# Kernel optimization log

Hardware: AMD Instinct MI355X
Metric: run time of the kernel (lower is better)

Reference implementation:

```python
import jax, jax.numpy as jnp
import numpy as np

N_NODES = 50000   # number of graph nodes
N_EDGES = 800000  # avg degree 16
D = 128           # in_dim == all hdims -> residual active every layer
L = 3             # len(cfg['hdims'])


def setup_inputs() -> dict:
    key = jax.random.key(0)
    ks = jax.random.split(key, 8)
    scale = 1.0 / np.sqrt(D)
    x = jax.random.normal(ks[0], (N_NODES, D), dtype=jnp.float32)
    edge_index = jax.random.randint(ks[1], (2, N_EDGES), 0, N_NODES, dtype=jnp.int32)
    in_fc_w = jax.random.normal(ks[2], (D, D), dtype=jnp.float32) * scale
    in_fc_b = jnp.zeros((D,), dtype=jnp.float32)
    # GraphConv per layer: lin_rel (with bias) applied to aggregated neighbors,
    # lin_root (no bias) applied to self features. All layers are DxD -> stack.
    w_rel = jax.random.normal(ks[3], (L, D, D), dtype=jnp.float32) * scale
    b_rel = jnp.zeros((L, D), dtype=jnp.float32)
    w_root = jax.random.normal(ks[4], (L, D, D), dtype=jnp.float32) * scale
    return {"x": x, "edge_index": edge_index, "in_fc_w": in_fc_w,
            "in_fc_b": in_fc_b, "w_rel": w_rel, "b_rel": b_rel, "w_root": w_root}


def reference(x, edge_index, in_fc_w, in_fc_b, w_rel, b_rel, w_root):
    src, dst = edge_index[0], edge_index[1]
    h = x @ in_fc_w + in_fc_b                     # in_fc
    for l in range(L):                            # fixed small layer count
        # GraphConv, aggr='add': gather source feats, scatter-add to targets
        agg = jax.ops.segment_sum(h[src], dst, num_segments=N_NODES)  # [N, D]
        out = agg @ w_rel[l] + b_rel[l] + h @ w_root[l]
        out = jax.nn.relu(out)
        h = out + h                               # residual (dims match)
    return h
```

## Files before the change

### kernel.cpp

```cpp
#include <hip/hip_runtime.h>
#include <hip/hip_bf16.h>


constexpr int D = 128;
constexpr int NB_SHIFT = 7;
constexpr int BCAP = 2560;
constexpr int STRIDE = 3456;
constexpr int CHUNK = 2048;
constexpr int NRANGE = 16;

typedef __attribute__((ext_vector_type(8))) short bf16x8;
typedef __attribute__((ext_vector_type(4))) float f32x4;
typedef __attribute__((ext_vector_type(4))) unsigned int u32x4;

__device__ inline unsigned short f2bf(float f) {
    unsigned int u = __builtin_bit_cast(unsigned int, f);
    u += 0x7FFFu + ((u >> 16) & 1u);
    return (unsigned short)(u >> 16);
}
__device__ inline float bf2f(unsigned short v) {
    return __builtin_bit_cast(float, (unsigned int)v << 16);
}
__device__ inline float bf2f_lo(unsigned int v) {
    return __builtin_bit_cast(float, v << 16);
}
__device__ inline float bf2f_hi(unsigned int v) {
    return __builtin_bit_cast(float, v & 0xFFFF0000u);
}

__global__ __launch_bounds__(256) void prep(
    const float* __restrict__ x, const float* __restrict__ fc_w,
    const float* __restrict__ w_rel, const float* __restrict__ w_root,
    unsigned short* __restrict__ xb, unsigned short* __restrict__ Wp,
    int* __restrict__ cursor, unsigned short* __restrict__ hb0,
    unsigned short* __restrict__ hb1, int n4, int NB, int N)
{
    int blk = blockIdx.x;
    const int nconv = (n4 + 255) / 256;
    if (blk < nconv) {
        int i = blk * 256 + threadIdx.x;
        if (i < n4) {
            float4 v = ((const float4*)x)[i];
            ushort4 o;
            o.x = f2bf(v.x); o.y = f2bf(v.y); o.z = f2bf(v.z); o.w = f2bf(v.w);
            ((ushort4*)xb)[i] = o;
        }
        return;
    }
    blk -= nconv;
    if (blk < 56) {
        int idx = blk * 256 + threadIdx.x;
        int mat  = idx >> 11;
        int rem  = idx & 2047;
        int tn   = rem >> 8;
        int ks   = (rem >> 6) & 3;
        int lane = rem & 63;
        const float* w = (mat == 0) ? fc_w
                       : (mat <= 3) ? w_rel  + (size_t)(mat - 1) * D * D
                                    : w_root + (size_t)(mat - 4) * D * D;
        unsigned short* wp = Wp + (size_t)mat * D * D + (size_t)rem * 8;
        int kbase = ks * 32 + (lane >> 4) * 8;
        int col   = tn * 16 + (lane & 15);
        #pragma unroll
        for (int j = 0; j < 8; ++j)
            wp[j] = f2bf(w[(size_t)(kbase + j) * D + col]);
        return;
    }
    blk -= 56;
    const int ncb = (NB + 255) / 256;
    if (blk < ncb) {
        int i = blk * 256 + threadIdx.x;
        if (i < NB) cursor[i] = 0;
        return;
    }
    if (threadIdx.x < 64)
        ((unsigned int*)(hb0 + (size_t)N * D))[threadIdx.x] = 0u;
    else if (threadIdx.x < 128)
        ((unsigned int*)(hb1 + (size_t)N * D))[threadIdx.x - 64] = 0u;
}

__global__ __launch_bounds__(256) void gemm_mfma(
    const unsigned short* __restrict__ A1, const unsigned short* __restrict__ W1p,
    const float* __restrict__ bias, unsigned short* __restrict__ hb_out, int N)
{
    const int tid  = threadIdx.x;
    const int wave = tid >> 6;
    const int lane = tid & 63;
    const int row0 = blockIdx.x * 64 + wave * 16;
    const int mrow = lane & 15;
    const int kgrp = lane >> 4;

    f32x4 acc[8];
    #pragma unroll
    for (int t = 0; t < 8; ++t) acc[t] = (f32x4){0.f, 0.f, 0.f, 0.f};

    int arow = row0 + mrow; if (arow >= N) arow = N - 1;
    const size_t abase = (size_t)arow * D + kgrp * 8;

    #pragma unroll
    for (int ks = 0; ks < 4; ++ks) {
        bf16x8 a1 = *(const bf16x8*)(A1 + abase + ks * 32);
        #pragma unroll
        for (int tn = 0; tn < 8; ++tn) {
            bf16x8 b = *(const bf16x8*)(W1p + ((size_t)((tn * 4 + ks) * 64 + lane) * 8));
            acc[tn] = __builtin_amdgcn_mfma_f32_16x16x32_bf16(a1, b, acc[tn], 0, 0, 0);
        }
    }

    const int r0 = row0 + kgrp * 4;
    #pragma unroll
    for (int tn = 0; tn < 8; ++tn) {
        const int col = tn * 16 + mrow;
        const float bv = bias[col];
        #pragma unroll
        for (int reg = 0; reg < 4; ++reg) {
            int r = r0 + reg;
            if (r < N) hb_out[(size_t)r * D + col] = f2bf(acc[tn][reg] + bv);
        }
    }
}

__global__ __launch_bounds__(256) void layer_fused(
    const unsigned short* __restrict__ hb_in, const int* __restrict__ eb,
    const unsigned int* __restrict__ sorted_off,
    const unsigned short* __restrict__ Wrel, const unsigned short* __restrict__ Wroot,
    const float* __restrict__ bias,
    unsigned short* hb_out, float* out_f32, int N)
{
    __shared__ unsigned short aggt[16][136];

    const int tid   = threadIdx.x;
    const int wave  = tid >> 6;
    const int lane  = tid & 63;
    const int node0 = blockIdx.x * 16;

    {
        const int g = lane >> 4;
        const int c = lane & 15;
        const int n = node0 + wave * 4 + g;

        float acc[8];
        #pragma unroll
        for (int q = 0; q < 8; ++q) acc[q] = 0.f;

        if (n < N) {
            const int2 be = ((const int2*)eb)[n];
            int j = be.x;
            const int e = be.y;
            const unsigned int c16 = (unsigned int)c * 16u;
            const char* hb = (const char*)hb_in;
            if (j < e) {
                u32x4 iA = *(const u32x4*)(sorted_off + j);
                u32x4 iB = *(const u32x4*)(sorted_off + j + 4);
                for (;;) {
                    u32x4 v0 = *(const u32x4*)(hb + (iA[0] + c16));
                    u32x4 v1 = *(const u32x4*)(hb + (iA[1] + c16));
                    u32x4 v2 = *(const u32x4*)(hb + (iA[2] + c16));
                    u32x4 v3 = *(const u32x4*)(hb + (iA[3] + c16));
                    u32x4 v4 = *(const u32x4*)(hb + (iB[0] + c16));
                    u32x4 v5 = *(const u32x4*)(hb + (iB[1] + c16));
                    u32x4 v6 = *(const u32x4*)(hb + (iB[2] + c16));
                    u32x4 v7 = *(const u32x4*)(hb + (iB[3] + c16));
                    const bool more = (j + 8 < e);
                    u32x4 nA, nB;
                    if (more) {
                        nA = *(const u32x4*)(sorted_off + j + 8);
                        nB = *(const u32x4*)(sorted_off + j + 12);
                    }
                    #pragma unroll
                    for (int q = 0; q < 4; ++q) {
                        acc[2 * q]     += ((bf2f_lo(v0[q]) + bf2f_lo(v1[q])) + (bf2f_lo(v2[q]) + bf2f_lo(v3[q])))
                                        + ((bf2f_lo(v4[q]) + bf2f_lo(v5[q])) + (bf2f_lo(v6[q]) + bf2f_lo(v7[q])));
                        acc[2 * q + 1] += ((bf2f_hi(v0[q]) + bf2f_hi(v1[q])) + (bf2f_hi(v2[q]) + bf2f_hi(v3[q])))
                                        + ((bf2f_hi(v4[q]) + bf2f_hi(v5[q])) + (bf2f_hi(v6[q]) + bf2f_hi(v7[q])));
                    }
                    if (!more) break;
                    iA = nA; iB = nB; j += 8;
                }
            }
        }
        u32x4 o;
        #pragma unroll
        for (int q = 0; q < 4; ++q)
            o[q] = (unsigned int)f2bf(acc[2 * q]) |
                   ((unsigned int)f2bf(acc[2 * q + 1]) << 16);
        *(u32x4*)&aggt[wave * 4 + g][c * 8] = o;
    }
    __syncthreads();

    const int mrow = lane & 15;
    const int kgrp = lane >> 4;

    f32x4 acc2[2];
    acc2[0] = (f32x4){0.f, 0.f, 0.f, 0.f};
    acc2[1] = (f32x4){0.f, 0.f, 0.f, 0.f};

    int arow = node0 + mrow; if (arow >= N) arow = N - 1;
    const size_t abase = (size_t)arow * D + kgrp * 8;

    #pragma unroll
    for (int ks = 0; ks < 4; ++ks) {
        bf16x8 a1 = *(const bf16x8*)&aggt[mrow][ks * 32 + kgrp * 8];
        bf16x8 a2 = *(const bf16x8*)(hb_in + abase + ks * 32);
        #pragma unroll
        for (int t = 0; t < 2; ++t) {
            const int tn = wave * 2 + t;
            bf16x8 b1 = *(const bf16x8*)(Wrel  + ((size_t)((tn * 4 + ks) * 64 + lane) * 8));
            acc2[t] = __builtin_amdgcn_mfma_f32_16x16x32_bf16(a1, b1, acc2[t], 0, 0, 0);
            bf16x8 b2 = *(const bf16x8*)(Wroot + ((size_t)((tn * 4 + ks) * 64 + lane) * 8));
            acc2[t] = __builtin_amdgcn_mfma_f32_16x16x32_bf16(a2, b2, acc2[t], 0, 0, 0);
        }
    }

    const int r0 = node0 + kgrp * 4;
    #pragma unroll
    for (int t = 0; t < 2; ++t) {
        const int tn  = wave * 2 + t;
        const int col = tn * 16 + mrow;
        const float bv = bias[col];
        #pragma unroll
        for (int reg = 0; reg < 4; ++reg) {
            int r = r0 + reg;
            if (r < N) {
                float z = fmaxf(acc2[t][reg] + bv, 0.f);
                float o = z + bf2f(hb_in[(size_t)r * D + col]);
                if (out_f32 != nullptr) out_f32[(size_t)r * D + col] = o;
                else                    hb_out[(size_t)r * D + col] = f2bf(o);
            }
        }
    }
}

__global__ __launch_bounds__(256) void bucket_scatter(
    const int* __restrict__ src, const int* __restrict__ dst,
    unsigned int* __restrict__ entries, int* __restrict__ cursor, int E, int NB)
{
    __shared__ unsigned int   stage[CHUNK];
    __shared__ unsigned short bslot[CHUNK];
    __shared__ int lhist[512];
    __shared__ int lscan[512];
    __shared__ int lgbase[512];
    __shared__ int lcur[512];
    __shared__ int sh[256];

    const int base  = blockIdx.x * CHUNK;
    const int count = min(CHUNK, E - base);
    const int tid   = threadIdx.x;

    for (int i = tid; i < 512; i += 256) { lhist[i] = 0; lcur[i] = 0; }
    __syncthreads();

    for (int i = tid; i < count; i += 256)
        atomicAdd(&lhist[dst[base + i] >> NB_SHIFT], 1);
    __syncthreads();

    int v2 = lhist[2 * tid] + lhist[2 * tid + 1];
    sh[tid] = v2;
    __syncthreads();
    #pragma unroll
    for (int off = 1; off < 256; off <<= 1) {
        int t = (tid >= off) ? sh[tid - off] : 0;
        __syncthreads();
        sh[tid] += t;
        __syncthreads();
    }
    int excl2 = sh[tid] - v2;
    lscan[2 * tid]     = excl2;
    lscan[2 * tid + 1] = excl2 + lhist[2 * tid];
    __syncthreads();

    for (int t = tid; t < 512; t += 256) {
        int c = (t < NB) ? lhist[t] : 0;
        lgbase[t] = (c > 0) ? atomicAdd(&cursor[t], c) : 0;
    }
    __syncthreads();

    for (int i = tid; i < count; i += 256) {
        int d = dst[base + i];
        int s = src[base + i];
        int b = d >> NB_SHIFT;
        int p = atomicAdd(&lcur[b], 1);
        int slot = lscan[b] + p;
        stage[slot] = ((unsigned int)(d & ((1 << NB_SHIFT) - 1)) << 16) | (unsigned int)s;
        bslot[slot] = (unsigned short)b;
    }
    __syncthreads();

    for (int i = tid; i < count; i += 256) {
        int b   = bslot[i];
        int off = i - lscan[b] + lgbase[b];
        if (off < BCAP) entries[(size_t)b * BCAP + off] = stage[i];
    }
}

__global__ __launch_bounds__(256) void bucket_sort(
    const unsigned int* __restrict__ entries, const int* __restrict__ cursor,
    unsigned int* __restrict__ sorted_off, int* __restrict__ eb,
    int N, int NB, float inv_range, unsigned int zero_off)
{
    const int b   = blockIdx.x;
    const int tid = threadIdx.x;

    __shared__ int nhist[128 * NRANGE];
    __shared__ int nscan[128 * NRANGE];
    __shared__ int ncur[128 * NRANGE];
    __shared__ int nbase[129];
    __shared__ int sh[256];
    __shared__ unsigned int svals[STRIDE];

    const int cnt = min(cursor[b], BCAP);

    for (int i = tid; i < 128 * NRANGE; i += 256) { nhist[i] = 0; ncur[i] = 0; }
    __syncthreads();

    const unsigned int* ebase = entries + (size_t)b * BCAP;
    for (int i = tid; i < cnt; i += 256) {
        unsigned int e = ebase[i];
        int s = (int)(e & 0xFFFFu);
        int r = (int)((float)s * inv_range); if (r > NRANGE - 1) r = NRANGE - 1;
        atomicAdd(&nhist[(int)((e >> 16) << 4) | r], 1);
    }
    __syncthreads();

    int c4 = 0, pc = 0;
    if (tid < 128) {
        int s = 0;
        #pragma unroll
        for (int q = 0; q < NRANGE; ++q) s += nhist[NRANGE * tid + q];
        c4 = s;
        pc = (c4 + 7) & ~7;
    }
    sh[tid] = (tid < 128) ? pc : 0;
    __syncthreads();
    #pragma unroll
    for (int off = 1; off < 128; off <<= 1) {
        int t = (tid >= off && tid < 128) ? sh[tid - off] : 0;
        __syncthreads();
        if (tid < 128) sh[tid] += t;
        __syncthreads();
    }
    if (tid < 128) nbase[tid] = sh[tid] - pc;
    if (tid == 127) nbase[128] = sh[127];
    __syncthreads();
    const int padded_total = nbase[128];

    if (tid < 128) {
        int base = nbase[tid];
        int run = base;
        #pragma unroll
        for (int q = 0; q < NRANGE; ++q) {
            nscan[NRANGE * tid + q] = run;
            run += nhist[NRANGE * tid + q];
        }
        int nn = (b << NB_SHIFT) + tid;
        if (nn < N) {
            eb[2 * nn]     = b * STRIDE + base;
            eb[2 * nn + 1] = b * STRIDE + base + pc;
        }
    }
    for (int i = tid; i < padded_total; i += 256) svals[i] = zero_off;
    __syncthreads();

    for (int i = tid; i < cnt; i += 256) {
        unsigned int e = ebase[i];
        int s = (int)(e & 0xFFFFu);
        int r = (int)((float)s * inv_range); if (r > NRANGE - 1) r = NRANGE - 1;
        int key = (int)((e >> 16) << 4) | r;
        int p = atomicAdd(&ncur[key], 1);
        svals[nscan[key] + p] = ((unsigned int)s) << 8;
    }
    __syncthreads();

    unsigned int* obase = sorted_off + (size_t)b * STRIDE;
    for (int i = tid; i < padded_total; i += 256) obase[i] = svals[i];
}

extern "C" void kernel_launch(void* const* d_in, const int* in_sizes, int n_in,
                              void* d_out, int out_size, void* d_ws, size_t ws_size,
                              hipStream_t stream)
{
    const float* x      = (const float*)d_in[0];
    const int*   ei     = (const int*)  d_in[1];
    const float* fc_w   = (const float*)d_in[2];
    const float* fc_b   = (const float*)d_in[3];
    const float* w_rel  = (const float*)d_in[4];
    const float* b_rel  = (const float*)d_in[5];
    const float* w_root = (const float*)d_in[6];
    float* out = (float*)d_out;

    const int N = in_sizes[0] / D;
    const int E = in_sizes[1] / 2;
    const int* src = ei;
    const int* dst = ei + E;
    const int NB = (N + (1 << NB_SHIFT) - 1) >> NB_SHIFT;

    char* p = (char*)d_ws;
    unsigned short* hb0 = (unsigned short*)p;  p += (size_t)(N + 1) * D * sizeof(unsigned short);
    unsigned short* hb1 = (unsigned short*)p;  p += (size_t)(N + 1) * D * sizeof(unsigned short);
    unsigned short* Wp  = (unsigned short*)p;  p += (size_t)7 * D * D * sizeof(unsigned short);
    unsigned int* sorted_off = (unsigned int*)p;  p += (size_t)NB * STRIDE * sizeof(unsigned int);
    int* eb     = (int*)p;                     p += (size_t)2 * N * sizeof(int);
    int* cursor = (int*)p;                     p += (size_t)NB * sizeof(int);
    unsigned int* entries = (unsigned int*)d_out;

    unsigned short* Wp_in   = Wp;
    unsigned short* Wp_rel  = Wp + (size_t)1 * D * D;
    unsigned short* Wp_root = Wp + (size_t)4 * D * D;
    unsigned short* xb = hb1;

    const int n4 = N * D / 4;
    const int gemm_blocks  = (N + 63) / 64;
    const int layer_blocks = (N + 15) / 16;
    const int prep_blocks  = (n4 + 255) / 256 + 56 + (NB + 255) / 256 + 1;

    prep<<<prep_blocks, 256, 0, stream>>>(x, fc_w, w_rel, w_root, xb, Wp, cursor,
                                          hb0, hb1, n4, NB, N);

    bucket_scatter<<<(E + CHUNK - 1) / CHUNK, 256, 0, stream>>>(
        src, dst, entries, cursor, E, NB);
    bucket_sort<<<NB, 256, 0, stream>>>(
        entries, cursor, sorted_off, eb, N, NB, (float)NRANGE / (float)N,
        ((unsigned int)N) << 8);

    gemm_mfma<<<gemm_blocks, 256, 0, stream>>>(xb, Wp_in, fc_b, hb0, N);

    unsigned short* hin  = hb0;
    unsigned short* hout = hb1;
    for (int l = 0; l < 3; ++l) {
        layer_fused<<<layer_blocks, 256, 0, stream>>>(
            hin, eb, sorted_off,
            Wp_rel + (size_t)l * D * D, Wp_root + (size_t)l * D * D,
            b_rel + (size_t)l * D,
            (l == 2) ? nullptr : hout,
            (l == 2) ? out : nullptr, N);
        unsigned short* t = hin; hin = hout; hout = t;
    }
}
```

Baseline: 238.3 us.

## Fuse input GEMM with edge bucket scatter and convert x to bf16 in-kernel

Removes the separate fp32-to-bf16 conversion pass over x from the prep kernel; the input GEMM now loads fp32 x directly and converts in registers. The GEMM is merged into the bucket_scatter launch as extra blocks, so the independent edge-bucketing and input projection run concurrently in one launch. This drops a full write and reread of the bf16 copy of x and one kernel launch. The merged kernel carries the scatter's shared-memory footprint in every block, which may lower occupancy for the GEMM blocks.

```diff
diff --git a/kernel.cpp b/kernel.cpp
--- a/kernel.cpp
+++ b/kernel.cpp
@@ -29,25 +29,12 @@
 }
 
 __global__ __launch_bounds__(256) void prep(
-    const float* __restrict__ x, const float* __restrict__ fc_w,
-    const float* __restrict__ w_rel, const float* __restrict__ w_root,
-    unsigned short* __restrict__ xb, unsigned short* __restrict__ Wp,
+    const float* __restrict__ fc_w, const float* __restrict__ w_rel,
+    const float* __restrict__ w_root, unsigned short* __restrict__ Wp,
     int* __restrict__ cursor, unsigned short* __restrict__ hb0,
-    unsigned short* __restrict__ hb1, int n4, int NB, int N)
+    unsigned short* __restrict__ hb1, int NB, int N)
 {
     int blk = blockIdx.x;
-    const int nconv = (n4 + 255) / 256;
-    if (blk < nconv) {
-        int i = blk * 256 + threadIdx.x;
-        if (i < n4) {
-            float4 v = ((const float4*)x)[i];
-            ushort4 o;
-            o.x = f2bf(v.x); o.y = f2bf(v.y); o.z = f2bf(v.z); o.w = f2bf(v.w);
-            ((ushort4*)xb)[i] = o;
-        }
-        return;
-    }
-    blk -= nconv;
     if (blk < 56) {
         int idx = blk * 256 + threadIdx.x;
         int mat  = idx >> 11;
@@ -79,14 +66,77 @@
         ((unsigned int*)(hb1 + (size_t)N * D))[threadIdx.x - 64] = 0u;
 }
 
-__global__ __launch_bounds__(256) void gemm_mfma(
-    const unsigned short* __restrict__ A1, const unsigned short* __restrict__ W1p,
+__global__ __launch_bounds__(256) void scatter_gemm(
+    const int* __restrict__ src, const int* __restrict__ dst,
+    unsigned int* __restrict__ entries, int* __restrict__ cursor, int E, int NB, int NS,
+    const float* __restrict__ x, const unsigned short* __restrict__ W1p,
     const float* __restrict__ bias, unsigned short* __restrict__ hb_out, int N)
 {
-    const int tid  = threadIdx.x;
+    const int tid = threadIdx.x;
+
+    if (blockIdx.x < (unsigned)NS) {
+        __shared__ unsigned int   stage[CHUNK];
+        __shared__ unsigned short bslot[CHUNK];
+        __shared__ int lhist[512];
+        __shared__ int lscan[512];
+        __shared__ int lgbase[512];
+        __shared__ int lcur[512];
+        __shared__ int sh[256];
+
+        const int base  = blockIdx.x * CHUNK;
+        const int count = min(CHUNK, E - base);
+
+        for (int i = tid; i < 512; i += 256) { lhist[i] = 0; lcur[i] = 0; }
+        __syncthreads();
+
+        for (int i = tid; i < count; i += 256)
+            atomicAdd(&lhist[dst[base + i] >> NB_SHIFT], 1);
+        __syncthreads();
+
+        int v2 = lhist[2 * tid] + lhist[2 * tid + 1];
+        sh[tid] = v2;
+        __syncthreads();
+        #pragma unroll
+        for (int off = 1; off < 256; off <<= 1) {
+            int t = (tid >= off) ? sh[tid - off] : 0;
+            __syncthreads();
+            sh[tid] += t;
+            __syncthreads();
+        }
+        int excl2 = sh[tid] - v2;
+        lscan[2 * tid]     = excl2;
+        lscan[2 * tid + 1] = excl2 + lhist[2 * tid];
+        __syncthreads();
+
+        for (int t = tid; t < 512; t += 256) {
+            int c = (t < NB) ? lhist[t] : 0;
+            lgbase[t] = (c > 0) ? atomicAdd(&cursor[t], c) : 0;
+        }
+        __syncthreads();
+
+        for (int i = tid; i < count; i += 256) {
+            int d = dst[base + i];
+            int s = src[base + i];
+            int b = d >> NB_SHIFT;
+            int p = atomicAdd(&lcur[b], 1);
+            int slot = lscan[b] + p;
+            stage[slot] = ((unsigned int)(d & ((1 << NB_SHIFT) - 1)) << 16) | (unsigned int)s;
+            bslot[slot] = (unsigned short)b;
+        }
+        __syncthreads();
+
+        for (int i = tid; i < count; i += 256) {
+            int b   = bslot[i];
+            int off = i - lscan[b] + lgbase[b];
+            if (off < BCAP) entries[(size_t)b * BCAP + off] = stage[i];
+        }
+        return;
+    }
+
+    const int blk  = blockIdx.x - NS;
     const int wave = tid >> 6;
     const int lane = tid & 63;
-    const int row0 = blockIdx.x * 64 + wave * 16;
+    const int row0 = blk * 64 + wave * 16;
     const int mrow = lane & 15;
     const int kgrp = lane >> 4;
 
@@ -95,11 +145,17 @@
     for (int t = 0; t < 8; ++t) acc[t] = (f32x4){0.f, 0.f, 0.f, 0.f};
 
     int arow = row0 + mrow; if (arow >= N) arow = N - 1;
-    const size_t abase = (size_t)arow * D + kgrp * 8;
+    const float* xr = x + (size_t)arow * D + kgrp * 8;
 
     #pragma unroll
     for (int ks = 0; ks < 4; ++ks) {
-        bf16x8 a1 = *(const bf16x8*)(A1 + abase + ks * 32);
+        float4 f0 = *(const float4*)(xr + ks * 32);
+        float4 f1 = *(const float4*)(xr + ks * 32 + 4);
+        bf16x8 a1;
+        a1[0] = (short)f2bf(f0.x); a1[1] = (short)f2bf(f0.y);
+        a1[2] = (short)f2bf(f0.z); a1[3] = (short)f2bf(f0.w);
+        a1[4] = (short)f2bf(f1.x); a1[5] = (short)f2bf(f1.y);
+        a1[6] = (short)f2bf(f1.z); a1[7] = (short)f2bf(f1.w);
         #pragma unroll
         for (int tn = 0; tn < 8; ++tn) {
             bf16x8 b = *(const bf16x8*)(W1p + ((size_t)((tn * 4 + ks) * 64 + lane) * 8));
@@ -118,6 +174,88 @@
             if (r < N) hb_out[(size_t)r * D + col] = f2bf(acc[tn][reg] + bv);
         }
     }
+}
+
+__global__ __launch_bounds__(256) void bucket_sort(
+    const unsigned int* __restrict__ entries, const int* __restrict__ cursor,
+    unsigned int* __restrict__ sorted_off, int* __restrict__ eb,
+    int N, int NB, float inv_range, unsigned int zero_off)
+{
+    const int b   = blockIdx.x;
+    const int tid = threadIdx.x;
+
+    __shared__ int nhist[128 * NRANGE];
+    __shared__ int nscan[128 * NRANGE];
+    __shared__ int ncur[128 * NRANGE];
+    __shared__ int nbase[129];
+    __shared__ int sh[256];
+    __shared__ unsigned int svals[STRIDE];
+
+    const int cnt = min(cursor[b], BCAP);
+
+    for (int i = tid; i < 128 * NRANGE; i += 256) { nhist[i] = 0; ncur[i] = 0; }
+    __syncthreads();
+
+    const unsigned int* ebase = entries + (size_t)b * BCAP;
+    for (int i = tid; i < cnt; i += 256) {
+        unsigned int e = ebase[i];
+        int s = (int)(e & 0xFFFFu);
+        int r = (int)((float)s * inv_range); if (r > NRANGE - 1) r = NRANGE - 1;
+        atomicAdd(&nhist[(int)((e >> 16) << 4) | r], 1);
+    }
+    __syncthreads();
+
+    int c4 = 0, pc = 0;
+    if (tid < 128) {
+        int s = 0;
+        #pragma unroll
+        for (int q = 0; q < NRANGE; ++q) s += nhist[NRANGE * tid + q];
+        c4 = s;
+        pc = (c4 + 7) & ~7;
+    }
+    sh[tid] = (tid < 128) ? pc : 0;
+    __syncthreads();
+    #pragma unroll
+    for (int off = 1; off < 128; off <<= 1) {
+        int t = (tid >= off && tid < 128) ? sh[tid - off] : 0;
+        __syncthreads();
+        if (tid < 128) sh[tid] += t;
+        __syncthreads();
+    }
+    if (tid < 128) nbase[tid] = sh[tid] - pc;
+    if (tid == 127) nbase[128] = sh[127];
+    __syncthreads();
+    const int padded_total = nbase[128];
+
+    if (tid < 128) {
+        int base = nbase[tid];
+        int run = base;
+        #pragma unroll
+        for (int q = 0; q < NRANGE; ++q) {
+            nscan[NRANGE * tid + q] = run;
+            run += nhist[NRANGE * tid + q];
+        }
+        int nn = (b << NB_SHIFT) + tid;
+        if (nn < N) {
+            eb[2 * nn]     = b * STRIDE + base;
+            eb[2 * nn + 1] = b * STRIDE + base + pc;
+        }
+    }
+    for (int i = tid; i < padded_total; i += 256) svals[i] = zero_off;
+    __syncthreads();
+
+    for (int i = tid; i < cnt; i += 256) {
+        unsigned int e = ebase[i];
+        int s = (int)(e & 0xFFFFu);
+        int r = (int)((float)s * inv_range); if (r > NRANGE - 1) r = NRANGE - 1;
+        int key = (int)((e >> 16) << 4) | r;
+        int p = atomicAdd(&ncur[key], 1);
+        svals[nscan[key] + p] = ((unsigned int)s) << 8;
+    }
+    __syncthreads();
+
+    unsigned int* obase = sorted_off + (size_t)b * STRIDE;
+    for (int i = tid; i < padded_total; i += 256) obase[i] = svals[i];
 }
 
 __global__ __launch_bounds__(256) void layer_fused(
@@ -231,150 +369,6 @@
     }
 }
 
-__global__ __launch_bounds__(256) void bucket_scatter(
-    const int* __restrict__ src, const int* __restrict__ dst,
-    unsigned int* __restrict__ entries, int* __restrict__ cursor, int E, int NB)
-{
-    __shared__ unsigned int   stage[CHUNK];
-    __shared__ unsigned short bslot[CHUNK];
-    __shared__ int lhist[512];
-    __shared__ int lscan[512];
-    __shared__ int lgbase[512];
-    __shared__ int lcur[512];
-    __shared__ int sh[256];
-
-    const int base  = blockIdx.x * CHUNK;
-    const int count = min(CHUNK, E - base);
-    const int tid   = threadIdx.x;
-
-    for (int i = tid; i < 512; i += 256) { lhist[i] = 0; lcur[i] = 0; }
-    __syncthreads();
-
-    for (int i = tid; i < count; i += 256)
-        atomicAdd(&lhist[dst[base + i] >> NB_SHIFT], 1);
-    __syncthreads();
-
-    int v2 = lhist[2 * tid] + lhist[2 * tid + 1];
-    sh[tid] = v2;
-    __syncthreads();
-    #pragma unroll
-    for (int off = 1; off < 256; off <<= 1) {
-        int t = (tid >= off) ? sh[tid - off] : 0;
-        __syncthreads();
-        sh[tid] += t;
-        __syncthreads();
-    }
-    int excl2 = sh[tid] - v2;
-    lscan[2 * tid]     = excl2;
-    lscan[2 * tid + 1] = excl2 + lhist[2 * tid];
-    __syncthreads();
-
-    for (int t = tid; t < 512; t += 256) {
-        int c = (t < NB) ? lhist[t] : 0;
-        lgbase[t] = (c > 0) ? atomicAdd(&cursor[t], c) : 0;
-    }
-    __syncthreads();
-
-    for (int i = tid; i < count; i += 256) {
-        int d = dst[base + i];
-        int s = src[base + i];
-        int b = d >> NB_SHIFT;
-        int p = atomicAdd(&lcur[b], 1);
-        int slot = lscan[b] + p;
-        stage[slot] = ((unsigned int)(d & ((1 << NB_SHIFT) - 1)) << 16) | (unsigned int)s;
-        bslot[slot] = (unsigned short)b;
-    }
-    __syncthreads();
-
-    for (int i = tid; i < count; i += 256) {
-        int b   = bslot[i];
-        int off = i - lscan[b] + lgbase[b];
-        if (off < BCAP) entries[(size_t)b * BCAP + off] = stage[i];
-    }
-}
-
-__global__ __launch_bounds__(256) void bucket_sort(
-    const unsigned int* __restrict__ entries, const int* __restrict__ cursor,
-    unsigned int* __restrict__ sorted_off, int* __restrict__ eb,
-    int N, int NB, float inv_range, unsigned int zero_off)
-{
-    const int b   = blockIdx.x;
-    const int tid = threadIdx.x;
-
-    __shared__ int nhist[128 * NRANGE];
-    __shared__ int nscan[128 * NRANGE];
-    __shared__ int ncur[128 * NRANGE];
-    __shared__ int nbase[129];
-    __shared__ int sh[256];
-    __shared__ unsigned int svals[STRIDE];
-
-    const int cnt = min(cursor[b], BCAP);
-
-    for (int i = tid; i < 128 * NRANGE; i += 256) { nhist[i] = 0; ncur[i] = 0; }
-    __syncthreads();
-
-    const unsigned int* ebase = entries + (size_t)b * BCAP;
-    for (int i = tid; i < cnt; i += 256) {
-        unsigned int e = ebase[i];
-        int s = (int)(e & 0xFFFFu);
-        int r = (int)((float)s * inv_range); if (r > NRANGE - 1) r = NRANGE - 1;
-        atomicAdd(&nhist[(int)((e >> 16) << 4) | r], 1);
-    }
-    __syncthreads();
-
-    int c4 = 0, pc = 0;
-    if (tid < 128) {
-        int s = 0;
-        #pragma unroll
-        for (int q = 0; q < NRANGE; ++q) s += nhist[NRANGE * tid + q];
-        c4 = s;
-        pc = (c4 + 7) & ~7;
-    }
-    sh[tid] = (tid < 128) ? pc : 0;
-    __syncthreads();
-    #pragma unroll
-    for (int off = 1; off < 128; off <<= 1) {
-        int t = (tid >= off && tid < 128) ? sh[tid - off] : 0;
-        __syncthreads();
-        if (tid < 128) sh[tid] += t;
-        __syncthreads();
-    }
-    if (tid < 128) nbase[tid] = sh[tid] - pc;
-    if (tid == 127) nbase[128] = sh[127];
-    __syncthreads();
-    const int padded_total = nbase[128];
-
-    if (tid < 128) {
-        int base = nbase[tid];
-        int run = base;
-        #pragma unroll
-        for (int q = 0; q < NRANGE; ++q) {
-            nscan[NRANGE * tid + q] = run;
-            run += nhist[NRANGE * tid + q];
-        }
-        int nn = (b << NB_SHIFT) + tid;
-        if (nn < N) {
-            eb[2 * nn]     = b * STRIDE + base;
-            eb[2 * nn + 1] = b * STRIDE + base + pc;
-        }
-    }
-    for (int i = tid; i < padded_total; i += 256) svals[i] = zero_off;
-    __syncthreads();
-
-    for (int i = tid; i < cnt; i += 256) {
-        unsigned int e = ebase[i];
-        int s = (int)(e & 0xFFFFu);
-        int r = (int)((float)s * inv_range); if (r > NRANGE - 1) r = NRANGE - 1;
-        int key = (int)((e >> 16) << 4) | r;
-        int p = atomicAdd(&ncur[key], 1);
-        svals[nscan[key] + p] = ((unsigned int)s) << 8;
-    }
-    __syncthreads();
-
-    unsigned int* obase = sorted_off + (size_t)b * STRIDE;
-    for (int i = tid; i < padded_total; i += 256) obase[i] = svals[i];
-}
-
 extern "C" void kernel_launch(void* const* d_in, const int* in_sizes, int n_in,
                               void* d_out, int out_size, void* d_ws, size_t ws_size,
                               hipStream_t stream)
@@ -406,23 +400,22 @@
     unsigned short* Wp_in   = Wp;
     unsigned short* Wp_rel  = Wp + (size_t)1 * D * D;
     unsigned short* Wp_root = Wp + (size_t)4 * D * D;
-    unsigned short* xb = hb1;
-
-    const int n4 = N * D / 4;
+
+    const int NS = (E + CHUNK - 1) / CHUNK;
     const int gemm_blocks  = (N + 63) / 64;
     const int layer_blocks = (N + 15) / 16;
-    const int prep_blocks  = (n4 + 255) / 256 + 56 + (NB + 255) / 256 + 1;
-
-    prep<<<prep_blocks, 256, 0, stream>>>(x, fc_w, w_rel, w_root, xb, Wp, cursor,
-                                          hb0, hb1, n4, NB, N);
-
-    bucket_scatter<<<(E + CHUNK - 1) / CHUNK, 256, 0, stream>>>(
-        src, dst, entries, cursor, E, NB);
+    const int prep_blocks  = 56 + (NB + 255) / 256 + 1;
+
+    prep<<<prep_blocks, 256, 0, stream>>>(fc_w, w_rel, w_root, Wp, cursor,
+                                          hb0, hb1, NB, N);
+
+    scatter_gemm<<<NS + gemm_blocks, 256, 0, stream>>>(
+        src, dst, entries, cursor, E, NB, NS,
+        x, Wp_in, fc_b, hb0, N);
+
     bucket_sort<<<NB, 256, 0, stream>>>(
         entries, cursor, sorted_off, eb, N, NB, (float)NRANGE / (float)N,
         ((unsigned int)N) << 8);
-
-    gemm_mfma<<<gemm_blocks, 256, 0, stream>>>(xb, Wp_in, fc_b, hb0, N);
 
     unsigned short* hin  = hb0;
     unsigned short* hout = hb1;
```

Result: faster. 229.5 us (-3.7%).
